# Performance work log

Hardware: AMD Instinct MI355X
Metric: run time of the kernel (lower is better)

The kernel has to match this reference:

```python
import jax, jax.numpy as jnp
import numpy as np

DIM = 1024
N_HEAD = 16
HEAD_DIM = DIM // N_HEAD
B, T = 4, 2048
NEG = -1e9


def setup_inputs() -> dict:
    key = jax.random.key(0)
    ks = jax.random.split(key, 5)
    x = jax.random.normal(ks[0], (B, T, DIM), dtype=jnp.float32)
    # additive causal mask, broadcast over batch and heads
    causal = jnp.triu(jnp.full((T, T), NEG, dtype=jnp.float32), k=1)
    mask = causal[None, None, :, :]  # [1,1,T,T]
    s = 1.0 / np.sqrt(DIM)
    wq = jax.random.normal(ks[1], (DIM, DIM), dtype=jnp.float32) * s
    wk = jax.random.normal(ks[2], (DIM, DIM), dtype=jnp.float32) * s
    wv = jax.random.normal(ks[3], (DIM, DIM), dtype=jnp.float32) * s
    wo = jax.random.normal(ks[4], (DIM, DIM), dtype=jnp.float32) * s
    return {"x": x, "mask": mask, "wq": wq, "wk": wk, "wv": wv, "wo": wo}


def reference(x, mask, wq, wk, wv, wo):
    Bn, Tn, C = x.shape
    # torch nn.Linear(dim,dim,bias=False): y = x @ W^T
    q = (x @ wq.T).reshape(Bn, Tn, N_HEAD, HEAD_DIM).transpose(0, 2, 1, 3)  # [B,H,T,D]
    k = (x @ wk.T).reshape(Bn, Tn, N_HEAD, HEAD_DIM).transpose(0, 2, 1, 3)
    v = (x @ wv.T).reshape(Bn, Tn, N_HEAD, HEAD_DIM).transpose(0, 2, 1, 3)
    scale = 1.0 / np.sqrt(HEAD_DIM).astype(np.float32)
    attn = jnp.einsum('bhqd,bhkd->bhqk', q, k) * scale  # [B,H,T,T]
    attn = attn + mask
    attn = jax.nn.softmax(attn, axis=-1)
    out = jnp.einsum('bhqk,bhkd->bhqd', attn, v)  # [B,H,T,D]
    out = out.transpose(0, 2, 1, 3).reshape(Bn, Tn, C)
    return out @ wo.T
```

## Files before the change

### kernel.cpp

```cpp
#include <hip/hip_runtime.h>
#include <hip/hip_bf16.h>

typedef __attribute__((ext_vector_type(8))) short short8;
typedef __attribute__((ext_vector_type(4))) short short4v;
typedef __attribute__((ext_vector_type(4))) float float4v;

#define DIM   1024
#define NH    16
#define HD    64
#define BSZ   4
#define TSZ   2048
#define BT    (BSZ*TSZ)

#define PSTR  72

#define SBIAS 24.0f

typedef const __attribute__((address_space(1))) void* gptr_t;
typedef __attribute__((address_space(3))) void* lptr_t;

__device__ __forceinline__ short f2bs(float x) {
    __hip_bfloat16 h = __float2bfloat16(x);
    return __builtin_bit_cast(short, h);
}

__global__ __launch_bounds__(256) void cvt_kernel(
    const float* __restrict__ x,  const float* __restrict__ wq,
    const float* __restrict__ wk, const float* __restrict__ wv,
    const float* __restrict__ wo,
    __hip_bfloat16* __restrict__ xb,  __hip_bfloat16* __restrict__ wqb,
    __hip_bfloat16* __restrict__ wkb, __hip_bfloat16* __restrict__ wvb,
    __hip_bfloat16* __restrict__ wob)
{
    int bid = blockIdx.x;
    const float* src; __hip_bfloat16* dst; int base;
    if (bid < 8192) { src = x; dst = xb; base = bid; }
    else {
        int wsel = (bid - 8192) >> 10;
        base = (bid - 8192) & 1023;
        src = (wsel == 0) ? wq : (wsel == 1) ? wk : (wsel == 2) ? wv : wo;
        dst = (wsel == 0) ? wqb : (wsel == 1) ? wkb : (wsel == 2) ? wvb : wob;
    }
    size_t off = (size_t)base * 1024 + threadIdx.x * 4;
    float4v v = *(const float4v*)(src + off);
    short4v o;
    o[0] = f2bs(v[0]); o[1] = f2bs(v[1]); o[2] = f2bs(v[2]); o[3] = f2bs(v[3]);
    *(short4v*)((short*)dst + off) = o;
}

__device__ __forceinline__ void gemm_core(
    const __hip_bfloat16* __restrict__ A,
    const __hip_bfloat16* __restrict__ B,
    __hip_bfloat16* smA, __hip_bfloat16* smB,
    int m0, int n0, int tid, float4v acc[4][4])
{
    const int wid = tid >> 6, lane = tid & 63;
    const int quad = lane >> 4, l15 = lane & 15;
    const int l7 = l15 & 7;
    const int wm = (wid >> 1) * 64, wn = (wid & 1) * 64;
    const int srow = tid >> 3;
    const int scol = ((tid & 7) ^ (srow & 7)) * 8;

    const __hip_bfloat16* gA0 = A + (size_t)(m0 + srow) * DIM + scol;
    const __hip_bfloat16* gB0 = B + (size_t)(n0 + srow) * DIM + scol;

    for (int kc = 0; kc < DIM; kc += 64) {
        __syncthreads();
#pragma unroll
        for (int j = 0; j < 4; j++) {
            __builtin_amdgcn_global_load_lds((gptr_t)(gA0 + (size_t)(j*32)*DIM + kc),
                (lptr_t)(smA + j*2048 + tid*8), 16, 0, 0);
            __builtin_amdgcn_global_load_lds((gptr_t)(gB0 + (size_t)(j*32)*DIM + kc),
                (lptr_t)(smB + j*2048 + tid*8), 16, 0, 0);
        }
        __syncthreads();

#pragma unroll
        for (int s = 0; s < 2; s++) {
            short8 a[4], b[4];
#pragma unroll
            for (int mb = 0; mb < 4; mb++)
                a[mb] = *(const short8*)(smA + (wm + mb*16 + l15)*64 + ((s*4 + quad) ^ l7)*8);
#pragma unroll
            for (int nb = 0; nb < 4; nb++)
                b[nb] = *(const short8*)(smB + (wn + nb*16 + l15)*64 + ((s*4 + quad) ^ l7)*8);
#pragma unroll
            for (int mb = 0; mb < 4; mb++)
#pragma unroll
                for (int nb = 0; nb < 4; nb++)
                    acc[mb][nb] = __builtin_amdgcn_mfma_f32_16x16x32_bf16(
                        a[mb], b[nb], acc[mb][nb], 0, 0, 0);
        }
    }
}

__global__ __launch_bounds__(256) void qkv_gemm(
    const __hip_bfloat16* __restrict__ xb,
    const __hip_bfloat16* __restrict__ wqb,
    const __hip_bfloat16* __restrict__ wkb,
    const __hip_bfloat16* __restrict__ wvb,
    __hip_bfloat16* __restrict__ Qb,
    __hip_bfloat16* __restrict__ Kb,
    __hip_bfloat16* __restrict__ Vt)
{
    __shared__ __hip_bfloat16 smA[128*64];
    __shared__ __hip_bfloat16 smB[128*64];

    const int z = blockIdx.z;
    const __hip_bfloat16* w = (z == 0) ? wqb : ((z == 1) ? wkb : wvb);
    const int tid = threadIdx.x;
    const int wid = tid >> 6, lane = tid & 63;
    const int quad = lane >> 4, l15 = lane & 15;
    const int m0 = blockIdx.x * 128, n0 = blockIdx.y * 128;
    const int wm0 = m0 + (wid >> 1) * 64;
    const int wn0 = n0 + (wid & 1) * 64;
    const float qscale = 0.1803368801111204f;

    float4v acc[4][4];
#pragma unroll
    for (int i = 0; i < 4; i++)
#pragma unroll
        for (int j = 0; j < 4; j++)
#pragma unroll
            for (int r = 0; r < 4; r++) acc[i][j][r] = 0.0f;

    gemm_core(xb, w, smA, smB, m0, n0, tid, acc);

    if (z == 2) {
        const int h = wn0 >> 6;
#pragma unroll
        for (int mb = 0; mb < 4; mb++) {
            int m = wm0 + mb*16 + quad*4;
            int bb = m >> 11, t0 = m & 2047;
#pragma unroll
            for (int nb = 0; nb < 4; nb++) {
                int d = nb*16 + l15;
                short4v pk;
                pk[0] = f2bs(acc[mb][nb][0]); pk[1] = f2bs(acc[mb][nb][1]);
                pk[2] = f2bs(acc[mb][nb][2]); pk[3] = f2bs(acc[mb][nb][3]);
                *(short4v*)(Vt + (size_t)((bb*NH + h)*HD + d)*TSZ + t0) = pk;
            }
        }
    } else {
        const float sc = (z == 0) ? qscale : 1.0f;
        __hip_bfloat16* dst = (z == 0) ? Qb : Kb;
#pragma unroll
        for (int mb = 0; mb < 4; mb++)
#pragma unroll
            for (int r = 0; r < 4; r++) {
                int m = wm0 + mb*16 + quad*4 + r;
                int bb = m >> 11, t = m & 2047;
#pragma unroll
                for (int nb = 0; nb < 4; nb++) {
                    int n = wn0 + nb*16 + l15;
                    int h = n >> 6, d = n & 63;
                    dst[(size_t)((bb*NH + h)*TSZ + t)*HD + d] =
                        __float2bfloat16(acc[mb][nb][r] * sc);
                }
            }
    }
}

__global__ __launch_bounds__(256, 2) void attn(
    const __hip_bfloat16* __restrict__ Qb,
    const __hip_bfloat16* __restrict__ Kb,
    const __hip_bfloat16* __restrict__ Vt,
    __hip_bfloat16* __restrict__ Ob)
{
    __shared__ __hip_bfloat16 smK[64*64];
    __shared__ __hip_bfloat16 smV[64*64];
    __shared__ __hip_bfloat16 Pl[4][32*PSTR];

    const int qperm[16] = {15,14,13,12,8,9,10,11,4,5,6,7,3,2,1,0};
    const int bh = blockIdx.x;
    const int qt = qperm[blockIdx.y];
    const int q0 = qt * 128;
    const int tid = threadIdx.x;
    const int wid = tid >> 6, lane = tid & 63;
    const int quad = lane >> 4, l15 = lane & 15;
    const int l7 = l15 & 7;
    const int q0w = q0 + wid * 32;

    const __hip_bfloat16* Qp = Qb + (size_t)bh * TSZ * HD;
    const __hip_bfloat16* Kp = Kb + (size_t)bh * TSZ * HD;
    const __hip_bfloat16* Vp = Vt + (size_t)bh * HD * TSZ;
    __hip_bfloat16* P = &Pl[wid][0];

    const int srow = tid >> 3;
    const int scol = ((tid & 7) ^ (srow & 7)) * 8;

    short8 bq[2][2];
#pragma unroll
    for (int nt = 0; nt < 2; nt++)
#pragma unroll
        for (int c = 0; c < 2; c++)
            bq[nt][c] = *(const short8*)(Qp + (size_t)(q0w + nt*16 + l15)*HD + c*32 + quad*8);

    float lsum[2] = {0.f, 0.f};
    float4v ot[4][2];
#pragma unroll
    for (int mt = 0; mt < 4; mt++)
#pragma unroll
        for (int nt = 0; nt < 2; nt++)
#pragma unroll
            for (int r = 0; r < 4; r++) ot[mt][nt][r] = 0.f;

    const int ntb = 2*qt + 2;
    for (int it = 0; it < ntb; ++it) {
        const int k0 = it * 64;

        __syncthreads();
#pragma unroll
        for (int c = 0; c < 2; c++) {
            __builtin_amdgcn_global_load_lds(
                (gptr_t)(Kp + (size_t)(k0 + srow + 32*c)*HD + scol),
                (lptr_t)(smK + tid*8 + c*2048), 16, 0, 0);
            __builtin_amdgcn_global_load_lds(
                (gptr_t)(Vp + (size_t)(srow + 32*c)*TSZ + k0 + scol),
                (lptr_t)(smV + tid*8 + c*2048), 16, 0, 0);
        }
        __syncthreads();

        if (k0 > q0w + 31) continue;

        float4v st[4][2];
#pragma unroll
        for (int mt = 0; mt < 4; mt++)
#pragma unroll
            for (int nt = 0; nt < 2; nt++)
#pragma unroll
                for (int r = 0; r < 4; r++) st[mt][nt][r] = 0.f;
#pragma unroll
        for (int c = 0; c < 2; c++)
#pragma unroll
            for (int mt = 0; mt < 4; mt++) {
                short8 ak = *(const short8*)(smK + (mt*16 + l15)*64 + ((c*4 + quad) ^ l7)*8);
                st[mt][0] = __builtin_amdgcn_mfma_f32_16x16x32_bf16(ak, bq[0][c], st[mt][0], 0, 0, 0);
                st[mt][1] = __builtin_amdgcn_mfma_f32_16x16x32_bf16(ak, bq[1][c], st[mt][1], 0, 0, 0);
            }

        if (k0 + 63 > q0w) {
#pragma unroll
            for (int mt = 0; mt < 4; mt++)
#pragma unroll
                for (int nt = 0; nt < 2; nt++) {
                    int qn = q0w + nt*16 + l15;
#pragma unroll
                    for (int r = 0; r < 4; r++) {
                        int kg = k0 + mt*16 + quad*4 + r;
                        if (kg > qn) st[mt][nt][r] = -1e30f;
                    }
                }
        }

#pragma unroll
        for (int nt = 0; nt < 2; nt++) {
            float rs = 0.f;
#pragma unroll
            for (int mt = 0; mt < 4; mt++) {
                float p0 = exp2f(st[mt][nt][0] - SBIAS);
                float p1 = exp2f(st[mt][nt][1] - SBIAS);
                float p2 = exp2f(st[mt][nt][2] - SBIAS);
                float p3 = exp2f(st[mt][nt][3] - SBIAS);
                rs += (p0 + p1) + (p2 + p3);
                short4v pk;
                pk[0] = f2bs(p0); pk[1] = f2bs(p1);
                pk[2] = f2bs(p2); pk[3] = f2bs(p3);
                *(short4v*)(P + (nt*16 + l15)*PSTR + mt*16 + quad*4) = pk;
            }
            rs += __shfl_xor(rs, 16);
            rs += __shfl_xor(rs, 32);
            lsum[nt] += rs;
        }

        short8 bp[2][2];
#pragma unroll
        for (int nt = 0; nt < 2; nt++)
#pragma unroll
            for (int c2 = 0; c2 < 2; c2++)
                bp[nt][c2] = *(const short8*)(P + (nt*16 + l15)*PSTR + c2*32 + quad*8);

#pragma unroll
        for (int c2 = 0; c2 < 2; c2++)
#pragma unroll
            for (int mt = 0; mt < 4; mt++) {
                short8 av = *(const short8*)(smV + (mt*16 + l15)*64 + ((c2*4 + quad) ^ l7)*8);
                ot[mt][0] = __builtin_amdgcn_mfma_f32_16x16x32_bf16(av, bp[0][c2], ot[mt][0], 0, 0, 0);
                ot[mt][1] = __builtin_amdgcn_mfma_f32_16x16x32_bf16(av, bp[1][c2], ot[mt][1], 0, 0, 0);
            }
    }

    const int b = bh >> 4, h = bh & 15;
#pragma unroll
    for (int nt = 0; nt < 2; nt++) {
        const float inv = 1.0f / lsum[nt];
        const int qn = q0w + nt*16 + l15;
        const size_t rowbase = (size_t)((b*TSZ + qn)*NH + h) * HD;
#pragma unroll
        for (int mt = 0; mt < 4; mt++) {
            short4v pk;
            pk[0] = f2bs(ot[mt][nt][0] * inv); pk[1] = f2bs(ot[mt][nt][1] * inv);
            pk[2] = f2bs(ot[mt][nt][2] * inv); pk[3] = f2bs(ot[mt][nt][3] * inv);
            *(short4v*)(Ob + rowbase + mt*16 + quad*4) = pk;
        }
    }
}

__global__ __launch_bounds__(256) void out_gemm(
    const __hip_bfloat16* __restrict__ A,
    const __hip_bfloat16* __restrict__ w,
    float* __restrict__ out)
{
    __shared__ __hip_bfloat16 smA[128*64];
    __shared__ __hip_bfloat16 smB[128*64];

    const int tid = threadIdx.x;
    const int wid = tid >> 6, lane = tid & 63;
    const int quad = lane >> 4, l15 = lane & 15;
    const int m0 = blockIdx.x * 128, n0 = blockIdx.y * 128;
    const int wm0 = m0 + (wid >> 1) * 64;
    const int wn0 = n0 + (wid & 1) * 64;

    float4v acc[4][4];
#pragma unroll
    for (int i = 0; i < 4; i++)
#pragma unroll
        for (int j = 0; j < 4; j++)
#pragma unroll
            for (int r = 0; r < 4; r++) acc[i][j][r] = 0.0f;

    gemm_core(A, w, smA, smB, m0, n0, tid, acc);

#pragma unroll
    for (int mb = 0; mb < 4; mb++)
#pragma unroll
        for (int nb = 0; nb < 4; nb++)
#pragma unroll
            for (int r = 0; r < 4; r++) {
                int m = wm0 + mb*16 + quad*4 + r;
                int n = wn0 + nb*16 + l15;
                out[(size_t)m*DIM + n] = acc[mb][nb][r];
            }
}

extern "C" void kernel_launch(void* const* d_in, const int* in_sizes, int n_in,
                              void* d_out, int out_size, void* d_ws, size_t ws_size,
                              hipStream_t stream) {
    const float* x  = (const float*)d_in[0];
    const float* wq = (const float*)d_in[2];
    const float* wk = (const float*)d_in[3];
    const float* wv = (const float*)d_in[4];
    const float* wo = (const float*)d_in[5];
    float* out = (float*)d_out;

    char* ws = (char*)d_ws;
    const size_t MB = (size_t)1024 * 1024;
    __hip_bfloat16* Qb  = (__hip_bfloat16*)(ws);
    __hip_bfloat16* Kb  = (__hip_bfloat16*)(ws + 16*MB);
    __hip_bfloat16* Vt  = (__hip_bfloat16*)(ws + 32*MB);
    __hip_bfloat16* xb  = (__hip_bfloat16*)(ws + 48*MB);
    __hip_bfloat16* Ob  = (__hip_bfloat16*)(ws + 48*MB);
    __hip_bfloat16* wqb = (__hip_bfloat16*)(ws + 64*MB);
    __hip_bfloat16* wkb = (__hip_bfloat16*)(ws + 66*MB);
    __hip_bfloat16* wvb = (__hip_bfloat16*)(ws + 68*MB);
    __hip_bfloat16* wob = (__hip_bfloat16*)(ws + 70*MB);

    dim3 blk(256);
    cvt_kernel<<<dim3(8192 + 4*1024), blk, 0, stream>>>(
        x, wq, wk, wv, wo, xb, wqb, wkb, wvb, wob);
    qkv_gemm<<<dim3(BT/128, DIM/128, 3), blk, 0, stream>>>(
        xb, wqb, wkb, wvb, Qb, Kb, Vt);
    attn<<<dim3(BSZ*NH, 16), blk, 0, stream>>>(Qb, Kb, Vt, Ob);
    out_gemm<<<dim3(BT/128, DIM/128), blk, 0, stream>>>(Ob, wob, out);
}
```

Baseline: 250.9 us.

## Double-buffer K/V tiles in LDS and fold softmax bias into accumulator init

Adds a second LDS buffer for the K and V tiles. The next tile is prefetched with global_load_lds while the current one is being processed, which leaves one barrier per iteration instead of two. The constant softmax bias is also folded into the initial value of the score accumulator, removing one subtraction per exp2. LDS use per block roughly doubles for K/V. The compiler may still insert conservative vmcnt waits before LDS reads, which would limit the overlap.

```diff
diff --git a/kernel.cpp b/kernel.cpp
--- a/kernel.cpp
+++ b/kernel.cpp
@@ -167,8 +167,8 @@
     const __hip_bfloat16* __restrict__ Vt,
     __hip_bfloat16* __restrict__ Ob)
 {
-    __shared__ __hip_bfloat16 smK[64*64];
-    __shared__ __hip_bfloat16 smV[64*64];
+    __shared__ __hip_bfloat16 smK[2][64*64];
+    __shared__ __hip_bfloat16 smV[2][64*64];
     __shared__ __hip_bfloat16 Pl[4][32*PSTR];
 
     const int qperm[16] = {15,14,13,12,8,9,10,11,4,5,6,7,3,2,1,0};
@@ -206,35 +206,53 @@
             for (int r = 0; r < 4; r++) ot[mt][nt][r] = 0.f;
 
     const int ntb = 2*qt + 2;
-    for (int it = 0; it < ntb; ++it) {
+
+#pragma unroll
+    for (int c = 0; c < 2; c++) {
+        __builtin_amdgcn_global_load_lds(
+            (gptr_t)(Kp + (size_t)(srow + 32*c)*HD + scol),
+            (lptr_t)(&smK[0][0] + tid*8 + c*2048), 16, 0, 0);
+        __builtin_amdgcn_global_load_lds(
+            (gptr_t)(Vp + (size_t)(srow + 32*c)*TSZ + scol),
+            (lptr_t)(&smV[0][0] + tid*8 + c*2048), 16, 0, 0);
+    }
+
+    int cur = 0;
+    for (int it = 0; it < ntb; ++it, cur ^= 1) {
         const int k0 = it * 64;
 
         __syncthreads();
-#pragma unroll
-        for (int c = 0; c < 2; c++) {
-            __builtin_amdgcn_global_load_lds(
-                (gptr_t)(Kp + (size_t)(k0 + srow + 32*c)*HD + scol),
-                (lptr_t)(smK + tid*8 + c*2048), 16, 0, 0);
-            __builtin_amdgcn_global_load_lds(
-                (gptr_t)(Vp + (size_t)(srow + 32*c)*TSZ + k0 + scol),
-                (lptr_t)(smV + tid*8 + c*2048), 16, 0, 0);
-        }
-        __syncthreads();
+
+        if (it + 1 < ntb) {
+            const int kn = k0 + 64;
+#pragma unroll
+            for (int c = 0; c < 2; c++) {
+                __builtin_amdgcn_global_load_lds(
+                    (gptr_t)(Kp + (size_t)(kn + srow + 32*c)*HD + scol),
+                    (lptr_t)(&smK[cur^1][0] + tid*8 + c*2048), 16, 0, 0);
+                __builtin_amdgcn_global_load_lds(
+                    (gptr_t)(Vp + (size_t)(srow + 32*c)*TSZ + kn + scol),
+                    (lptr_t)(&smV[cur^1][0] + tid*8 + c*2048), 16, 0, 0);
+            }
+        }
 
         if (k0 > q0w + 31) continue;
 
+        const __hip_bfloat16* sK = &smK[cur][0];
+        const __hip_bfloat16* sV = &smV[cur][0];
+
         float4v st[4][2];
 #pragma unroll
         for (int mt = 0; mt < 4; mt++)
 #pragma unroll
             for (int nt = 0; nt < 2; nt++)
 #pragma unroll
-                for (int r = 0; r < 4; r++) st[mt][nt][r] = 0.f;
+                for (int r = 0; r < 4; r++) st[mt][nt][r] = -SBIAS;
 #pragma unroll
         for (int c = 0; c < 2; c++)
 #pragma unroll
             for (int mt = 0; mt < 4; mt++) {
-                short8 ak = *(const short8*)(smK + (mt*16 + l15)*64 + ((c*4 + quad) ^ l7)*8);
+                short8 ak = *(const short8*)(sK + (mt*16 + l15)*64 + ((c*4 + quad) ^ l7)*8);
                 st[mt][0] = __builtin_amdgcn_mfma_f32_16x16x32_bf16(ak, bq[0][c], st[mt][0], 0, 0, 0);
                 st[mt][1] = __builtin_amdgcn_mfma_f32_16x16x32_bf16(ak, bq[1][c], st[mt][1], 0, 0, 0);
             }
@@ -258,10 +276,10 @@
             float rs = 0.f;
 #pragma unroll
             for (int mt = 0; mt < 4; mt++) {
-                float p0 = exp2f(st[mt][nt][0] - SBIAS);
-                float p1 = exp2f(st[mt][nt][1] - SBIAS);
-                float p2 = exp2f(st[mt][nt][2] - SBIAS);
-                float p3 = exp2f(st[mt][nt][3] - SBIAS);
+                float p0 = exp2f(st[mt][nt][0]);
+                float p1 = exp2f(st[mt][nt][1]);
+                float p2 = exp2f(st[mt][nt][2]);
+                float p3 = exp2f(st[mt][nt][3]);
                 rs += (p0 + p1) + (p2 + p3);
                 short4v pk;
                 pk[0] = f2bs(p0); pk[1] = f2bs(p1);
@@ -284,7 +302,7 @@
         for (int c2 = 0; c2 < 2; c2++)
 #pragma unroll
             for (int mt = 0; mt < 4; mt++) {
-                short8 av = *(const short8*)(smV + (mt*16 + l15)*64 + ((c2*4 + quad) ^ l7)*8);
+                short8 av = *(const short8*)(sV + (mt*16 + l15)*64 + ((c2*4 + quad) ^ l7)*8);
                 ot[mt][0] = __builtin_amdgcn_mfma_f32_16x16x32_bf16(av, bp[0][c2], ot[mt][0], 0, 0, 0);
                 ot[mt][1] = __builtin_amdgcn_mfma_f32_16x16x32_bf16(av, bp[1][c2], ot[mt][1], 0, 0, 0);
             }
```

New measurement: 252.8 us. No clear change (+0.8%).

## Halve attention query tile to 64 rows and raise occupancy to four blocks

Applied to the files above, without the earlier changes.

The attention kernel now processes 64 query rows per block, 16 per wave, instead of 128, with twice as many blocks, launch bounds raised for four blocks per CU, and a plain reverse block order in place of the permutation table. The softmax bias is folded into the MFMA accumulator initial value, and the causal mask is applied only on the last key tile. This aims for better load balance over the triangular workload and more latency hiding through occupancy. The cost is that each K/V tile loaded into LDS is reused by half as many queries, so K/V traffic doubles, and each wave issues fewer MFMAs per sync.

```diff
diff --git a/kernel.cpp b/kernel.cpp
--- a/kernel.cpp
+++ b/kernel.cpp
@@ -161,7 +161,7 @@
     }
 }
 
-__global__ __launch_bounds__(256, 2) void attn(
+__global__ __launch_bounds__(256, 4) void attn(
     const __hip_bfloat16* __restrict__ Qb,
     const __hip_bfloat16* __restrict__ Kb,
     const __hip_bfloat16* __restrict__ Vt,
@@ -169,17 +169,17 @@
 {
     __shared__ __hip_bfloat16 smK[64*64];
     __shared__ __hip_bfloat16 smV[64*64];
-    __shared__ __hip_bfloat16 Pl[4][32*PSTR];
-
-    const int qperm[16] = {15,14,13,12,8,9,10,11,4,5,6,7,3,2,1,0};
+    __shared__ __hip_bfloat16 Pl[4][16*PSTR];
+
     const int bh = blockIdx.x;
-    const int qt = qperm[blockIdx.y];
-    const int q0 = qt * 128;
+    const int qb = 31 - blockIdx.y;
+    const int q0 = qb * 64;
     const int tid = threadIdx.x;
     const int wid = tid >> 6, lane = tid & 63;
     const int quad = lane >> 4, l15 = lane & 15;
     const int l7 = l15 & 7;
-    const int q0w = q0 + wid * 32;
+    const int q0w = q0 + wid * 16;
+    const int qg  = q0w + l15;
 
     const __hip_bfloat16* Qp = Qb + (size_t)bh * TSZ * HD;
     const __hip_bfloat16* Kp = Kb + (size_t)bh * TSZ * HD;
@@ -189,23 +189,19 @@
     const int srow = tid >> 3;
     const int scol = ((tid & 7) ^ (srow & 7)) * 8;
 
-    short8 bq[2][2];
-#pragma unroll
-    for (int nt = 0; nt < 2; nt++)
-#pragma unroll
-        for (int c = 0; c < 2; c++)
-            bq[nt][c] = *(const short8*)(Qp + (size_t)(q0w + nt*16 + l15)*HD + c*32 + quad*8);
-
-    float lsum[2] = {0.f, 0.f};
-    float4v ot[4][2];
+    short8 bq[2];
+#pragma unroll
+    for (int c = 0; c < 2; c++)
+        bq[c] = *(const short8*)(Qp + (size_t)qg*HD + c*32 + quad*8);
+
+    float lsum = 0.f;
+    float4v ot[4];
 #pragma unroll
     for (int mt = 0; mt < 4; mt++)
 #pragma unroll
-        for (int nt = 0; nt < 2; nt++)
-#pragma unroll
-            for (int r = 0; r < 4; r++) ot[mt][nt][r] = 0.f;
-
-    const int ntb = 2*qt + 2;
+        for (int r = 0; r < 4; r++) ot[mt][r] = 0.f;
+
+    const int ntb = qb + 1;
     for (int it = 0; it < ntb; ++it) {
         const int k0 = it * 64;
 
@@ -221,88 +217,72 @@
         }
         __syncthreads();
 
-        if (k0 > q0w + 31) continue;
-
-        float4v st[4][2];
+        if (k0 > q0w + 15) continue;
+
+        float4v st[4];
 #pragma unroll
         for (int mt = 0; mt < 4; mt++)
 #pragma unroll
-            for (int nt = 0; nt < 2; nt++)
-#pragma unroll
-                for (int r = 0; r < 4; r++) st[mt][nt][r] = 0.f;
+            for (int r = 0; r < 4; r++) st[mt][r] = -SBIAS;
 #pragma unroll
         for (int c = 0; c < 2; c++)
 #pragma unroll
             for (int mt = 0; mt < 4; mt++) {
                 short8 ak = *(const short8*)(smK + (mt*16 + l15)*64 + ((c*4 + quad) ^ l7)*8);
-                st[mt][0] = __builtin_amdgcn_mfma_f32_16x16x32_bf16(ak, bq[0][c], st[mt][0], 0, 0, 0);
-                st[mt][1] = __builtin_amdgcn_mfma_f32_16x16x32_bf16(ak, bq[1][c], st[mt][1], 0, 0, 0);
-            }
-
-        if (k0 + 63 > q0w) {
+                st[mt] = __builtin_amdgcn_mfma_f32_16x16x32_bf16(ak, bq[c], st[mt], 0, 0, 0);
+            }
+
+        if (it == ntb - 1) {
 #pragma unroll
             for (int mt = 0; mt < 4; mt++)
 #pragma unroll
-                for (int nt = 0; nt < 2; nt++) {
-                    int qn = q0w + nt*16 + l15;
-#pragma unroll
-                    for (int r = 0; r < 4; r++) {
-                        int kg = k0 + mt*16 + quad*4 + r;
-                        if (kg > qn) st[mt][nt][r] = -1e30f;
-                    }
+                for (int r = 0; r < 4; r++) {
+                    int kg = k0 + mt*16 + quad*4 + r;
+                    if (kg > qg) st[mt][r] = -1e30f;
                 }
         }
 
-#pragma unroll
-        for (int nt = 0; nt < 2; nt++) {
-            float rs = 0.f;
-#pragma unroll
-            for (int mt = 0; mt < 4; mt++) {
-                float p0 = exp2f(st[mt][nt][0] - SBIAS);
-                float p1 = exp2f(st[mt][nt][1] - SBIAS);
-                float p2 = exp2f(st[mt][nt][2] - SBIAS);
-                float p3 = exp2f(st[mt][nt][3] - SBIAS);
-                rs += (p0 + p1) + (p2 + p3);
-                short4v pk;
-                pk[0] = f2bs(p0); pk[1] = f2bs(p1);
-                pk[2] = f2bs(p2); pk[3] = f2bs(p3);
-                *(short4v*)(P + (nt*16 + l15)*PSTR + mt*16 + quad*4) = pk;
-            }
-            rs += __shfl_xor(rs, 16);
-            rs += __shfl_xor(rs, 32);
-            lsum[nt] += rs;
-        }
-
-        short8 bp[2][2];
-#pragma unroll
-        for (int nt = 0; nt < 2; nt++)
-#pragma unroll
-            for (int c2 = 0; c2 < 2; c2++)
-                bp[nt][c2] = *(const short8*)(P + (nt*16 + l15)*PSTR + c2*32 + quad*8);
+        float rsm[4];
+#pragma unroll
+        for (int mt = 0; mt < 4; mt++) {
+            float p0 = exp2f(st[mt][0]);
+            float p1 = exp2f(st[mt][1]);
+            float p2 = exp2f(st[mt][2]);
+            float p3 = exp2f(st[mt][3]);
+            rsm[mt] = (p0 + p1) + (p2 + p3);
+            short4v pk;
+            pk[0] = f2bs(p0); pk[1] = f2bs(p1);
+            pk[2] = f2bs(p2); pk[3] = f2bs(p3);
+            *(short4v*)(P + l15*PSTR + mt*16 + quad*4) = pk;
+        }
+        float rs = (rsm[0] + rsm[1]) + (rsm[2] + rsm[3]);
+        rs += __shfl_xor(rs, 16);
+        rs += __shfl_xor(rs, 32);
+        lsum += rs;
+
+        short8 bp[2];
+#pragma unroll
+        for (int c2 = 0; c2 < 2; c2++)
+            bp[c2] = *(const short8*)(P + l15*PSTR + c2*32 + quad*8);
 
 #pragma unroll
         for (int c2 = 0; c2 < 2; c2++)
 #pragma unroll
             for (int mt = 0; mt < 4; mt++) {
                 short8 av = *(const short8*)(smV + (mt*16 + l15)*64 + ((c2*4 + quad) ^ l7)*8);
-                ot[mt][0] = __builtin_amdgcn_mfma_f32_16x16x32_bf16(av, bp[0][c2], ot[mt][0], 0, 0, 0);
-                ot[mt][1] = __builtin_amdgcn_mfma_f32_16x16x32_bf16(av, bp[1][c2], ot[mt][1], 0, 0, 0);
+                ot[mt] = __builtin_amdgcn_mfma_f32_16x16x32_bf16(av, bp[c2], ot[mt], 0, 0, 0);
             }
     }
 
     const int b = bh >> 4, h = bh & 15;
-#pragma unroll
-    for (int nt = 0; nt < 2; nt++) {
-        const float inv = 1.0f / lsum[nt];
-        const int qn = q0w + nt*16 + l15;
-        const size_t rowbase = (size_t)((b*TSZ + qn)*NH + h) * HD;
-#pragma unroll
-        for (int mt = 0; mt < 4; mt++) {
-            short4v pk;
-            pk[0] = f2bs(ot[mt][nt][0] * inv); pk[1] = f2bs(ot[mt][nt][1] * inv);
-            pk[2] = f2bs(ot[mt][nt][2] * inv); pk[3] = f2bs(ot[mt][nt][3] * inv);
-            *(short4v*)(Ob + rowbase + mt*16 + quad*4) = pk;
-        }
+    const float inv = 1.0f / lsum;
+    const size_t rowbase = (size_t)((b*TSZ + qg)*NH + h) * HD;
+#pragma unroll
+    for (int mt = 0; mt < 4; mt++) {
+        short4v pk;
+        pk[0] = f2bs(ot[mt][0] * inv); pk[1] = f2bs(ot[mt][1] * inv);
+        pk[2] = f2bs(ot[mt][2] * inv); pk[3] = f2bs(ot[mt][3] * inv);
+        *(short4v*)(Ob + rowbase + mt*16 + quad*4) = pk;
     }
 }
 
@@ -370,6 +350,6 @@
         x, wq, wk, wv, wo, xb, wqb, wkb, wvb, wob);
     qkv_gemm<<<dim3(BT/128, DIM/128, 3), blk, 0, stream>>>(
         xb, wqb, wkb, wvb, Qb, Kb, Vt);
-    attn<<<dim3(BSZ*NH, 16), blk, 0, stream>>>(Qb, Kb, Vt, Ob);
+    attn<<<dim3(BSZ*NH, 32), blk, 0, stream>>>(Qb, Kb, Vt, Ob);
     out_gemm<<<dim3(BT/128, DIM/128), blk, 0, stream>>>(Ob, wob, out);
 }
```

Result: no change. 255.2 us (+1.7%).
